# Kernel optimization log

Hardware: AMD Instinct MI355X
Metric: run time of the kernel (lower is better)

## Reference

```python
import jax, jax.numpy as jnp
import numpy as np

N = 100000     # total points
PBS = 500      # point_batch_size (hard-coded in module)
K = 100        # num_neighbors
KP = 15        # num_kernel_points
EPS = 1e-5


def _bn(x, g, b, axes):
    # torch BatchNorm in training mode: batch stats, biased variance
    m = jnp.mean(x, axis=axes, keepdims=True)
    v = jnp.var(x, axis=axes, keepdims=True)
    return (x - m) / jnp.sqrt(v + EPS) * g + b


def setup_inputs() -> dict:
    key = jax.random.key(0)
    ks = jax.random.split(key, 16)
    rn = lambda k, sh, s=1.0: jax.random.normal(k, sh, jnp.float32) * s
    return {
        "pts": rn(ks[0], (N, 3)),
        "normal": rn(ks[1], (N, 3)),
        "kp_points": rn(ks[2], (KP, 3)),
        "kp_weights": rn(ks[3], (KP, 3, 128), 0.3),
        "kp_sigma": jnp.float32(1.0),
        "conv1_w": rn(ks[4], (1024, 128), 128 ** -0.5),
        "conv1_b": rn(ks[5], (1024,), 0.02),
        "bn1_g": jnp.ones((1024,), jnp.float32),
        "bn1_b": jnp.zeros((1024,), jnp.float32),
        "fc1_w": rn(ks[6], (512, 1024), 1024 ** -0.5),
        "fc1_b": rn(ks[7], (512,), 0.02),
        "bn4_g": jnp.ones((512,), jnp.float32),
        "bn4_b": jnp.zeros((512,), jnp.float32),
        "fc2_w": rn(ks[8], (256, 512), 512 ** -0.5),
        "fc2_b": rn(ks[9], (256,), 0.02),
        "bn5_g": jnp.ones((256,), jnp.float32),
        "bn5_b": jnp.zeros((256,), jnp.float32),
        "fc3_w": rn(ks[10], (3, 256), 256 ** -0.5),
        "fc3_b": rn(ks[11], (3,), 0.02),
        "index": jax.random.randint(ks[12], (PBS,), 0, N, jnp.int32),
    }


def reference(pts, normal, kp_points, kp_weights, kp_sigma,
              conv1_w, conv1_b, bn1_g, bn1_b,
              fc1_w, fc1_b, bn4_g, bn4_b,
              fc2_w, fc2_b, bn5_g, bn5_b,
              fc3_w, fc3_b, index):
    sel = pts[index]                                               # [B,3]
    # L-inf pairwise distance and kNN (topk of -dist, as in the torch code)
    dist = jnp.max(jnp.abs(sel[:, None, :] - pts[None, :, :]), axis=-1)  # [B,N]
    _, nbr = jax.lax.top_k(-dist, K)                               # [B,K]
    rel = pts[nbr] - sel[:, None, :]                               # [B,K,3]

    # KPConv: gaussian weights vs kernel points, per-kernel-point linear map
    d2 = jnp.sum((rel[:, :, None, :] - kp_points[None, None]) ** 2, axis=-1)  # [B,K,KP]
    w = jnp.exp(-0.5 * d2 / (kp_sigma ** 2))
    wf = rel[:, :, None, :] * w[..., None]                         # [B,K,KP,3]
    h = jax.nn.relu(jnp.einsum('bnkc,kco->bno', wf, kp_weights))   # [B,K,128]

    # 1x1 conv 128->1024, relu then BN over (batch, points) per channel
    h = jnp.einsum('bnc,oc->bno', h, conv1_w) + conv1_b            # [B,K,1024]
    h = _bn(jax.nn.relu(h), bn1_g, bn1_b, (0, 1))
    feat = jnp.max(h, axis=1)                                      # [B,1024]

    feat = _bn(jax.nn.relu(feat @ fc1_w.T + fc1_b), bn4_g, bn4_b, (0,))
    feat = _bn(jax.nn.relu(feat @ fc2_w.T + fc2_b), bn5_g, bn5_b, (0,))
    feat = feat @ fc3_w.T + fc3_b                                  # [B,3]
    return feat, normal[index]
```

## Files before the change

kernel.cpp:

```cpp
#include <hip/hip_runtime.h>
#include <hip/hip_fp16.h>

#define NPTS 100000
#define NB 500
#define KNN 100
#define KPN 15
#define C1 128
#define C2 1024
#define C3 512
#define C4 256

#define G 64
#define NCELLS (G * G * G)
#define GB 5.0f
#define GINVH ((float)G / (2.f * GB))
#define CAND_CAP 2048

typedef _Float16 half8 __attribute__((ext_vector_type(8)));
typedef float f32x4 __attribute__((ext_vector_type(4)));

__device__ __forceinline__ int cell_coord(float x) {
  int c = (int)floorf((x + GB) * GINVH);
  return min(max(c, 0), G - 1);
}
__device__ __forceinline__ int cell_of(float x, float y, float z) {
  return (cell_coord(x) << 12) | (cell_coord(y) << 6) | cell_coord(z);
}

__global__ __launch_bounds__(256) void prep_kernel(
    const float* __restrict__ pts, const float* __restrict__ normal,
    const int* __restrict__ index, const float* __restrict__ w1,
    const float* __restrict__ kpw, const float* __restrict__ fc1w,
    const float* __restrict__ fc2w, float* __restrict__ sel,
    float* __restrict__ out2, __half* __restrict__ wh,
    __half* __restrict__ kpwT_hi, __half* __restrict__ kpwT_lo,
    __half* __restrict__ fwhi, __half* __restrict__ fwlo,
    __half* __restrict__ f2whi, __half* __restrict__ f2wlo,
    unsigned* __restrict__ cnt) {
  int i = blockIdx.x * 256 + threadIdx.x;
  if (i < NB) {
    int ix = index[i];
    sel[i * 3 + 0] = pts[3 * ix + 0];
    sel[i * 3 + 1] = pts[3 * ix + 1];
    sel[i * 3 + 2] = pts[3 * ix + 2];
    out2[i * 3 + 0] = normal[3 * ix + 0];
    out2[i * 3 + 1] = normal[3 * ix + 1];
    out2[i * 3 + 2] = normal[3 * ix + 2];
  }
  if (i < C2 * C1) wh[i] = __float2half(w1[i]);
  if (i < 128 * 64) {
    int o = i >> 6, j = i & 63;
    float v = (j < 45) ? kpw[j * 128 + o] : 0.f;
    __half hi = __float2half_rn(v);
    kpwT_hi[i] = hi;
    kpwT_lo[i] = __float2half_rn(v - __half2float(hi));
  }
  if (i < C3 * C2) {
    float v = fc1w[i];
    __half hi = __float2half_rn(v);
    fwhi[i] = hi;
    fwlo[i] = __float2half_rn(v - __half2float(hi));
  }
  if (i < C4 * C3) {
    float v = fc2w[i];
    __half hi = __float2half_rn(v);
    f2whi[i] = hi;
    f2wlo[i] = __float2half_rn(v - __half2float(hi));
  }
  if (i < NPTS)
    atomicAdd(&cnt[cell_of(pts[3 * i], pts[3 * i + 1], pts[3 * i + 2])], 1u);
}

__global__ __launch_bounds__(256) void grid_scan1_kernel(
    const unsigned* __restrict__ cnt, unsigned* __restrict__ cursor,
    unsigned* __restrict__ chunktot) {
  const int tid = threadIdx.x;
  int base = blockIdx.x * 1024 + tid * 4;
  unsigned c0 = cnt[base], c1 = cnt[base + 1], c2 = cnt[base + 2],
           c3 = cnt[base + 3];
  unsigned tot = c0 + c1 + c2 + c3;
  __shared__ unsigned sb[256];
  sb[tid] = tot;
  __syncthreads();
  for (int off = 1; off < 256; off <<= 1) {
    unsigned add = (tid >= off) ? sb[tid - off] : 0u;
    __syncthreads();
    sb[tid] += add;
    __syncthreads();
  }
  unsigned excl = sb[tid] - tot;
  cursor[base] = excl;
  cursor[base + 1] = excl + c0;
  cursor[base + 2] = excl + c0 + c1;
  cursor[base + 3] = excl + c0 + c1 + c2;
  if (tid == 255) chunktot[blockIdx.x] = sb[255];
}

__global__ __launch_bounds__(256) void grid_scan2_kernel(
    const unsigned* __restrict__ chunktot, unsigned* __restrict__ chunkoff) {
  const int tid = threadIdx.x;
  unsigned v = chunktot[tid];
  __shared__ unsigned sb[256];
  sb[tid] = v;
  __syncthreads();
  for (int off = 1; off < 256; off <<= 1) {
    unsigned add = (tid >= off) ? sb[tid - off] : 0u;
    __syncthreads();
    sb[tid] += add;
    __syncthreads();
  }
  chunkoff[tid] = sb[tid] - v;
}

__global__ __launch_bounds__(256) void grid_scan3_kernel(
    unsigned* __restrict__ cursor, const unsigned* __restrict__ chunkoff) {
  unsigned off = chunkoff[blockIdx.x];
  int base = blockIdx.x * 1024 + threadIdx.x * 4;
#pragma unroll
  for (int j = 0; j < 4; ++j) cursor[base + j] += off;
}

__global__ __launch_bounds__(256) void grid_scatter_kernel(
    const float* __restrict__ pts, unsigned* __restrict__ cursor,
    float4* __restrict__ sorted) {
  int i = blockIdx.x * 256 + threadIdx.x;
  if (i >= NPTS) return;
  float x = pts[3 * i], y = pts[3 * i + 1], z = pts[3 * i + 2];
  unsigned pos = atomicAdd(&cursor[cell_of(x, y, z)], 1u);
  sorted[pos] = make_float4(x, y, z, __int_as_float(i));
}

__device__ __forceinline__ unsigned linf_bits(float px, float py, float pz,
                                              float sx, float sy, float sz) {
  float dx = fabsf(px - sx), dy = fabsf(py - sy), dz = fabsf(pz - sz);
  return __float_as_uint(fmaxf(fmaxf(dx, dy), dz));
}

__global__ __launch_bounds__(256) void knn_kernel(
    const float4* __restrict__ sorted, const unsigned* __restrict__ cnt,
    const unsigned* __restrict__ cursor,
    const float* __restrict__ sel, int* __restrict__ nbr) {
  const int b = blockIdx.x;
  const int tid = threadIdx.x;
  __shared__ unsigned cbits[CAND_CAP];
  __shared__ int cidx[CAND_CAP];
  __shared__ unsigned hist[4096];
  __shared__ unsigned scanbuf[256];
  __shared__ int s_total, s_m, s_mc, s_chunk;
  __shared__ unsigned s_excl, s_bub;

  const float qx = sel[b * 3 + 0], qy = sel[b * 3 + 1], qz = sel[b * 3 + 2];
  const int qcx = cell_coord(qx), qcy = cell_coord(qy), qcz = cell_coord(qz);

  if (tid == 0) s_total = 0;
  __syncthreads();
  int s = 1;
  int pxlo = 1, pxhi = 0, pylo = 1, pyhi = 0, pzlo = 1, pzhi = 0;
  int xlo, xhi, ylo, yhi, zlo, zhi;
  for (;;) {
    xlo = max(qcx - s, 0); xhi = min(qcx + s, G - 1);
    ylo = max(qcy - s, 0); yhi = min(qcy + s, G - 1);
    zlo = max(qcz - s, 0); zhi = min(qcz + s, G - 1);
    int nx = xhi - xlo + 1, ny = yhi - ylo + 1, nz = zhi - zlo + 1;
    int ncell = nx * ny * nz;
    unsigned local = 0;
    for (int ci = tid; ci < ncell; ci += 256) {
      int cz = ci % nz;
      int r = ci / nz;
      int cy = r % ny;
      int cx = r / ny;
      int ax = xlo + cx, ay = ylo + cy, az = zlo + cz;
      if (ax >= pxlo && ax <= pxhi && ay >= pylo && ay <= pyhi &&
          az >= pzlo && az <= pzhi)
        continue;
      local += cnt[(ax << 12) | (ay << 6) | az];
    }
#pragma unroll
    for (int off = 32; off; off >>= 1) local += __shfl_down(local, off);
    if ((tid & 63) == 0) atomicAdd(&s_total, (int)local);
    __syncthreads();
    if (s_total >= KNN || (xlo == 0 && ylo == 0 && zlo == 0 && xhi == G - 1 &&
                           yhi == G - 1 && zhi == G - 1))
      break;
    pxlo = xlo; pxhi = xhi; pylo = ylo; pyhi = yhi; pzlo = zlo; pzhi = zhi;
    ++s;
    __syncthreads();
  }

  if (tid == 0) s_m = 0;
  __syncthreads();
  {
    int nx = xhi - xlo + 1, ny = yhi - ylo + 1, nz = zhi - zlo + 1;
    int ncell = nx * ny * nz;
    for (int ci = tid; ci < ncell; ci += 256) {
      int cz = ci % nz;
      int r = ci / nz;
      int cy = r % ny;
      int cx = r / ny;
      int cell = ((xlo + cx) << 12) | ((ylo + cy) << 6) | (zlo + cz);
      unsigned end = cursor[cell];
      unsigned beg = end - cnt[cell];
      int k = (int)(end - beg);
      if (k > 0) {
        int e0 = atomicAdd(&s_m, k);
        for (unsigned p = beg; p < end; ++p, ++e0) {
          if (e0 < CAND_CAP) {
            float4 f = sorted[p];
            cbits[e0] = linf_bits(f.x, f.y, f.z, qx, qy, qz);
            cidx[e0] = __float_as_int(f.w);
          }
        }
      }
    }
  }
  __syncthreads();
  int m = s_m < CAND_CAP ? s_m : CAND_CAP;

  for (int j = tid; j < 4096; j += 256) hist[j] = 0;
  __syncthreads();
  for (int e = tid; e < m; e += 256) atomicAdd(&hist[cbits[e] >> 19], 1u);
  __syncthreads();
  unsigned csum = 0;
  {
    int c0 = tid * 16;
#pragma unroll
    for (int j = 0; j < 16; ++j) csum += hist[c0 + j];
  }
  scanbuf[tid] = csum;
  __syncthreads();
  for (int off = 1; off < 256; off <<= 1) {
    unsigned add = (tid >= off) ? scanbuf[tid - off] : 0u;
    __syncthreads();
    scanbuf[tid] += add;
    __syncthreads();
  }
  {
    unsigned incl = scanbuf[tid], excl = incl - csum;
    if (excl < KNN && KNN <= incl) {
      s_chunk = tid;
      s_excl = excl;
    }
  }
  __syncthreads();
  if (tid == 0) {
    unsigned cum = s_excl;
    int bin = s_chunk * 16;
    while (cum + hist[bin] < KNN) {
      cum += hist[bin];
      ++bin;
    }
    s_bub = (unsigned)(bin + 1) << 19;
  }
  __syncthreads();

  const unsigned bub = s_bub;
  const float dub = __uint_as_float(bub);
  if (tid == 0) s_mc = 0;
  __syncthreads();
  {
    int xlo2 = min(max((int)floorf((qx - dub + GB) * GINVH), 0), G - 1);
    int xhi2 = min(max((int)floorf((qx + dub + GB) * GINVH), 0), G - 1);
    int ylo2 = min(max((int)floorf((qy - dub + GB) * GINVH), 0), G - 1);
    int yhi2 = min(max((int)floorf((qy + dub + GB) * GINVH), 0), G - 1);
    int zlo2 = min(max((int)floorf((qz - dub + GB) * GINVH), 0), G - 1);
    int zhi2 = min(max((int)floorf((qz + dub + GB) * GINVH), 0), G - 1);
    int nx = xhi2 - xlo2 + 1, ny = yhi2 - ylo2 + 1, nz = zhi2 - zlo2 + 1;
    int ncell = nx * ny * nz;
    for (int ci = tid; ci < ncell; ci += 256) {
      int cz = ci % nz;
      int r = ci / nz;
      int cy = r % ny;
      int cx = r / ny;
      int cell = ((xlo2 + cx) << 12) | ((ylo2 + cy) << 6) | (zlo2 + cz);
      unsigned end = cursor[cell];
      unsigned beg = end - cnt[cell];
      for (unsigned p = beg; p < end; ++p) {
        float4 f = sorted[p];
        unsigned bits = linf_bits(f.x, f.y, f.z, qx, qy, qz);
        if (bits < bub) {
          int e = atomicAdd(&s_mc, 1);
          if (e < CAND_CAP) {
            cbits[e] = bits;
            cidx[e] = __float_as_int(f.w);
          }
        }
      }
    }
  }
  __syncthreads();
  int mc = s_mc < CAND_CAP ? s_mc : CAND_CAP;

  for (int c = tid; c < mc; c += 256) {
    unsigned bc = cbits[c];
    int ic = cidx[c];
    int rank = 0;
    for (int j = 0; j < mc; ++j) {
      unsigned bj = cbits[j];
      rank += (bj < bc || (bj == bc && cidx[j] < ic)) ? 1 : 0;
    }
    if (rank < KNN) nbr[b * KNN + rank] = ic;
  }
}

__global__ __launch_bounds__(512, 2) void kpconv_conv1_kernel(
    const float* __restrict__ pts, const float* __restrict__ sel,
    const int* __restrict__ nbr, const float* __restrict__ kp_points,
    const __half* __restrict__ kpwT_hi, const __half* __restrict__ kpwT_lo,
    const float* __restrict__ kp_sigma, const __half* __restrict__ wh,
    const float* __restrict__ bias, float* __restrict__ featmax,
    float* __restrict__ featmin, float* __restrict__ featsum,
    float* __restrict__ featsq) {
  const int b = blockIdx.x;
  const int tid = threadIdx.x;
  const int wave = tid >> 6, lane = tid & 63;
  const int lr = lane & 15, quad = lane >> 4;

  __shared__ __align__(16) char smem[71168];
  __half* As_hi = (__half*)smem;
  __half* As_lo = As_hi + 112 * 72;
  __half* Bs_hi = As_lo + 112 * 72;
  __half* Bs_lo = Bs_hi + 128 * 72;
  float* rel = (float*)(Bs_lo + 128 * 72);
  float* kpp = rel + 100 * 4;
  __half* Hs = (__half*)smem;

  for (int i = tid; i < 128 * 8; i += 512) {
    int row = i >> 3, seg = i & 7;
    *(float4*)&Bs_hi[row * 72 + seg * 8] =
        *(const float4*)&kpwT_hi[row * 64 + seg * 8];
    *(float4*)&Bs_lo[row * 72 + seg * 8] =
        *(const float4*)&kpwT_lo[row * 64 + seg * 8];
  }
  {
    float4 z = make_float4(0.f, 0.f, 0.f, 0.f);
    for (int i = tid; i < 112 * 8; i += 512) {
      int row = i >> 3, seg = i & 7;
      *(float4*)&As_hi[row * 72 + seg * 8] = z;
      *(float4*)&As_lo[row * 72 + seg * 8] = z;
    }
  }
  if (tid < 45) kpp[tid] = kp_points[tid];
  if (tid < 100) {
    int idx = nbr[b * KNN + tid];
    rel[tid * 4 + 0] = pts[3 * idx + 0] - sel[b * 3 + 0];
    rel[tid * 4 + 1] = pts[3 * idx + 1] - sel[b * 3 + 1];
    rel[tid * 4 + 2] = pts[3 * idx + 2] - sel[b * 3 + 2];
  }
  __syncthreads();

  const float sg = kp_sigma[0];
  const float inv2s2 = -0.5f / (sg * sg);
  for (int i = tid; i < 100 * KPN; i += 512) {
    int k = i / KPN, p = i - k * KPN;
    float rx = rel[k * 4 + 0] - kpp[p * 3 + 0];
    float ry = rel[k * 4 + 1] - kpp[p * 3 + 1];
    float rz = rel[k * 4 + 2] - kpp[p * 3 + 2];
    float w = expf(inv2s2 * (rx * rx + ry * ry + rz * rz));
#pragma unroll
    for (int c = 0; c < 3; ++c) {
      float a = rel[k * 4 + c] * w;
      __half hi = __float2half_rn(a);
      As_hi[k * 72 + p * 3 + c] = hi;
      As_lo[k * 72 + p * 3 + c] = __float2half_rn(a - __half2float(hi));
    }
  }
  __syncthreads();

  f32x4 acc1[7];
#pragma unroll
  for (int m = 0; m < 7; ++m) acc1[m] = (f32x4)(0.f);
#pragma unroll
  for (int s = 0; s < 2; ++s) {
    int boff = (wave * 16 + lr) * 72 + s * 32 + quad * 8;
    half8 bhi = *(const half8*)&Bs_hi[boff];
    half8 blo = *(const half8*)&Bs_lo[boff];
#pragma unroll
    for (int m = 0; m < 7; ++m) {
      int aoff = (m * 16 + lr) * 72 + s * 32 + quad * 8;
      half8 ahi = *(const half8*)&As_hi[aoff];
      half8 alo = *(const half8*)&As_lo[aoff];
      acc1[m] = __builtin_amdgcn_mfma_f32_16x16x32_f16(ahi, bhi, acc1[m], 0, 0, 0);
      acc1[m] = __builtin_amdgcn_mfma_f32_16x16x32_f16(ahi, blo, acc1[m], 0, 0, 0);
      acc1[m] = __builtin_amdgcn_mfma_f32_16x16x32_f16(alo, bhi, acc1[m], 0, 0, 0);
    }
  }
  __syncthreads();

  {
    int col = wave * 16 + lr;
#pragma unroll
    for (int m = 0; m < 7; ++m)
#pragma unroll
      for (int r = 0; r < 4; ++r) {
        int row = m * 16 + quad * 4 + r;
        Hs[row * 136 + col] = __float2half_rn(fmaxf(acc1[m][r], 0.f));
      }
  }
  __syncthreads();

  half8 afr[4][7];
#pragma unroll
  for (int s = 0; s < 4; ++s)
#pragma unroll
    for (int m = 0; m < 7; ++m)
      afr[s][m] = *(const half8*)&Hs[(m * 16 + lr) * 136 + s * 32 + quad * 8];

  const int wrow = wave * 16 + lr;
  half8 bcur[4];
#pragma unroll
  for (int s = 0; s < 4; ++s)
    bcur[s] = *(const half8*)&wh[wrow * 128 + s * 32 + quad * 8];

  for (int c = 0; c < 8; ++c) {
    half8 bnxt[4];
    if (c + 1 < 8) {
#pragma unroll
      for (int s = 0; s < 4; ++s)
        bnxt[s] = *(const half8*)&wh[((c + 1) * 128 + wrow) * 128 + s * 32 +
                                     quad * 8];
    }

    f32x4 acc2[7];
#pragma unroll
    for (int m = 0; m < 7; ++m) acc2[m] = (f32x4)(0.f);
#pragma unroll
    for (int s = 0; s < 4; ++s)
#pragma unroll
      for (int m = 0; m < 7; ++m)
        acc2[m] = __builtin_amdgcn_mfma_f32_16x16x32_f16(afr[s][m], bcur[s],
                                                         acc2[m], 0, 0, 0);

    {
      int col = c * 128 + wrow;
      float bv = bias[col];
      float pmax = -1e30f, pmin = 1e30f, psum = 0.f, psq = 0.f;
#pragma unroll
      for (int m = 0; m < 7; ++m)
#pragma unroll
        for (int r = 0; r < 4; ++r) {
          int row = m * 16 + quad * 4 + r;
          if (row < 100) {
            float y = fmaxf(acc2[m][r] + bv, 0.f);
            pmax = fmaxf(pmax, y);
            pmin = fminf(pmin, y);
            psum += y;
            psq += y * y;
          }
        }
      pmax = fmaxf(pmax, __shfl_xor(pmax, 16));
      pmax = fmaxf(pmax, __shfl_xor(pmax, 32));
      pmin = fminf(pmin, __shfl_xor(pmin, 16));
      pmin = fminf(pmin, __shfl_xor(pmin, 32));
      psum += __shfl_xor(psum, 16);
      psum += __shfl_xor(psum, 32);
      psq += __shfl_xor(psq, 16);
      psq += __shfl_xor(psq, 32);
      if (quad == 0) {
        featmax[b * C2 + col] = pmax;
        featmin[b * C2 + col] = pmin;
        featsum[b * C2 + col] = psum;
        featsq[b * C2 + col] = psq;
      }
    }
#pragma unroll
    for (int s = 0; s < 4; ++s) bcur[s] = bnxt[s];
  }
}

__global__ __launch_bounds__(256) void stats1_kernel(
    const float* __restrict__ featsum, const float* __restrict__ featsq,
    float* __restrict__ bnsum, float* __restrict__ bnsq) {
  int col = blockIdx.x * 256 + threadIdx.x;
  int r0 = blockIdx.y * 50;
  float s = 0.f, q = 0.f;
  for (int r = r0; r < r0 + 50; ++r) {
    s += featsum[r * C2 + col];
    q += featsq[r * C2 + col];
  }
  atomicAdd(&bnsum[col], s);
  atomicAdd(&bnsq[col], q);
}

__global__ __launch_bounds__(256) void bn1half_kernel(
    const float* __restrict__ featmax, const float* __restrict__ featmin,
    const float* __restrict__ bnsum, const float* __restrict__ bnsq,
    const float* __restrict__ g, const float* __restrict__ bb,
    __half* __restrict__ Xhi, __half* __restrict__ Xlo) {
  int idx = blockIdx.x * 256 + threadIdx.x;
  if (idx >= NB * C2) return;
  int o = idx & (C2 - 1);
  const float invn = 1.f / (float)(NB * KNN);
  float m = bnsum[o] * invn;
  float v = bnsq[o] * invn - m * m;
  float a = g[o] / sqrtf(v + 1e-5f);
  float x = (a >= 0.f) ? featmax[idx] : featmin[idx];
  float y = (x - m) * a + bb[o];
  __half hi = __float2half_rn(y);
  Xhi[idx] = hi;
  Xlo[idx] = __float2half_rn(y - __half2float(hi));
}

__global__ __launch_bounds__(256) void fc1_mfma_kernel(
    const __half* __restrict__ Xhi, const __half* __restrict__ Xlo,
    const __half* __restrict__ Whi, const __half* __restrict__ Wlo,
    const float* __restrict__ bias, float* __restrict__ yraw,
    float* __restrict__ s, float* __restrict__ sq) {
  const int r0 = blockIdx.x * 64;
  const int n0 = blockIdx.y * 64;
  const int tid = threadIdx.x;
  const int wave = tid >> 6, lane = tid & 63;
  const int lr = lane & 15, quad = lane >> 4;
  __shared__ __half Xs_hi[64 * 72], Xs_lo[64 * 72];
  __shared__ __half Ws_hi[64 * 72], Ws_lo[64 * 72];

  f32x4 acc[4];
#pragma unroll
  for (int m = 0; m < 4; ++m) acc[m] = (f32x4)(0.f);

  for (int kc = 0; kc < C2; kc += 64) {
    __syncthreads();
    for (int i = tid; i < 64 * 8; i += 256) {
      int row = i >> 3, seg = i & 7;
      int gr = r0 + row;
      float4 vhi = make_float4(0.f, 0.f, 0.f, 0.f), vlo = vhi;
      if (gr < NB) {
        vhi = *(const float4*)&Xhi[gr * C2 + kc + seg * 8];
        vlo = *(const float4*)&Xlo[gr * C2 + kc + seg * 8];
      }
      *(float4*)&Xs_hi[row * 72 + seg * 8] = vhi;
      *(float4*)&Xs_lo[row * 72 + seg * 8] = vlo;
      *(float4*)&Ws_hi[row * 72 + seg * 8] =
          *(const float4*)&Whi[(n0 + row) * C2 + kc + seg * 8];
      *(float4*)&Ws_lo[row * 72 + seg * 8] =
          *(const float4*)&Wlo[(n0 + row) * C2 + kc + seg * 8];
    }
    __syncthreads();

#pragma unroll
    for (int s2 = 0; s2 < 2; ++s2) {
      int boff = (wave * 16 + lr) * 72 + s2 * 32 + quad * 8;
      half8 bhi = *(const half8*)&Ws_hi[boff];
      half8 blo = *(const half8*)&Ws_lo[boff];
#pragma unroll
      for (int m = 0; m < 4; ++m) {
        int aoff = (m * 16 + lr) * 72 + s2 * 32 + quad * 8;
        half8 ahi = *(const half8*)&Xs_hi[aoff];
        half8 alo = *(const half8*)&Xs_lo[aoff];
        acc[m] = __builtin_amdgcn_mfma_f32_16x16x32_f16(ahi, bhi, acc[m], 0, 0, 0);
        acc[m] = __builtin_amdgcn_mfma_f32_16x16x32_f16(ahi, blo, acc[m], 0, 0, 0);
        acc[m] = __builtin_amdgcn_mfma_f32_16x16x32_f16(alo, bhi, acc[m], 0, 0, 0);
      }
    }
  }

  {
    int col = n0 + wave * 16 + lr;
    float bv = bias[col];
    float psum = 0.f, psq = 0.f;
#pragma unroll
    for (int m = 0; m < 4; ++m)
#pragma unroll
      for (int r = 0; r < 4; ++r) {
        int row = r0 + m * 16 + quad * 4 + r;
        if (row < NB) {
          float y = fmaxf(acc[m][r] + bv, 0.f);
          yraw[row * C3 + col] = y;
          psum += y;
          psq += y * y;
        }
      }
    psum += __shfl_xor(psum, 16);
    psum += __shfl_xor(psum, 32);
    psq += __shfl_xor(psq, 16);
    psq += __shfl_xor(psq, 32);
    if (quad == 0) {
      atomicAdd(&s[col], psum);
      atomicAdd(&sq[col], psq);
    }
  }
}

__global__ __launch_bounds__(256) void fc2_mfma_kernel(
    const float* __restrict__ x,
    const float* __restrict__ bnsum4, const float* __restrict__ bnsq4,
    const float* __restrict__ g, const float* __restrict__ bb,
    const __half* __restrict__ Whi, const __half* __restrict__ Wlo,
    const float* __restrict__ bias, float* __restrict__ yraw,
    float* __restrict__ s, float* __restrict__ sq) {
  const int r0 = blockIdx.x * 64;
  const int n0 = blockIdx.y * 64;
  const int tid = threadIdx.x;
  const int wave = tid >> 6, lane = tid & 63;
  const int lr = lane & 15, quad = lane >> 4;
  __shared__ __half Xs_hi[64 * 72], Xs_lo[64 * 72];
  __shared__ __half Ws_hi[64 * 72], Ws_lo[64 * 72];
  __shared__ float amul[C3], badd[C3];

  {
    const float invn = 1.f / (float)NB;
    for (int o = tid; o < C3; o += 256) {
      float m = bnsum4[o] * invn;
      float v = bnsq4[o] * invn - m * m;
      float a = g[o] / sqrtf(v + 1e-5f);
      amul[o] = a;
      badd[o] = bb[o] - m * a;
    }
  }

  f32x4 acc[4];
#pragma unroll
  for (int m = 0; m < 4; ++m) acc[m] = (f32x4)(0.f);

  for (int kc = 0; kc < C3; kc += 64) {
    __syncthreads();
    for (int i = tid; i < 64 * 8; i += 256) {
      int row = i >> 3, seg = i & 7;
      int gr = r0 + row;
      __half hbuf[8], lbuf[8];
      if (gr < NB) {
        float4 a0 = *(const float4*)&x[gr * C3 + kc + seg * 8];
        float4 a1 = *(const float4*)&x[gr * C3 + kc + seg * 8 + 4];
        float vals[8] = {a0.x, a0.y, a0.z, a0.w, a1.x, a1.y, a1.z, a1.w};
#pragma unroll
        for (int j = 0; j < 8; ++j) {
          int o = kc + seg * 8 + j;
          float y = vals[j] * amul[o] + badd[o];
          __half hi = __float2half_rn(y);
          hbuf[j] = hi;
          lbuf[j] = __float2half_rn(y - __half2float(hi));
        }
      } else {
#pragma unroll
        for (int j = 0; j < 8; ++j) {
          hbuf[j] = __float2half_rn(0.f);
          lbuf[j] = __float2half_rn(0.f);
        }
      }
      *(float4*)&Xs_hi[row * 72 + seg * 8] = *(float4*)hbuf;
      *(float4*)&Xs_lo[row * 72 + seg * 8] = *(float4*)lbuf;
      *(float4*)&Ws_hi[row * 72 + seg * 8] =
          *(const float4*)&Whi[(n0 + row) * C3 + kc + seg * 8];
      *(float4*)&Ws_lo[row * 72 + seg * 8] =
          *(const float4*)&Wlo[(n0 + row) * C3 + kc + seg * 8];
    }
    __syncthreads();

#pragma unroll
    for (int s2 = 0; s2 < 2; ++s2) {
      int boff = (wave * 16 + lr) * 72 + s2 * 32 + quad * 8;
      half8 bhi = *(const half8*)&Ws_hi[boff];
      half8 blo = *(const half8*)&Ws_lo[boff];
#pragma unroll
      for (int m = 0; m < 4; ++m) {
        int aoff = (m * 16 + lr) * 72 + s2 * 32 + quad * 8;
        half8 ahi = *(const half8*)&Xs_hi[aoff];
        half8 alo = *(const half8*)&Xs_lo[aoff];
        acc[m] = __builtin_amdgcn_mfma_f32_16x16x32_f16(ahi, bhi, acc[m], 0, 0, 0);
        acc[m] = __builtin_amdgcn_mfma_f32_16x16x32_f16(ahi, blo, acc[m], 0, 0, 0);
        acc[m] = __builtin_amdgcn_mfma_f32_16x16x32_f16(alo, bhi, acc[m], 0, 0, 0);
      }
    }
  }

  {
    int col = n0 + wave * 16 + lr;
    float bv = bias[col];
    float psum = 0.f, psq = 0.f;
#pragma unroll
    for (int m = 0; m < 4; ++m)
#pragma unroll
      for (int r = 0; r < 4; ++r) {
        int row = r0 + m * 16 + quad * 4 + r;
        if (row < NB) {
          float y = fmaxf(acc[m][r] + bv, 0.f);
          yraw[row * C4 + col] = y;
          psum += y;
          psq += y * y;
        }
      }
    psum += __shfl_xor(psum, 16);
    psum += __shfl_xor(psum, 32);
    psq += __shfl_xor(psq, 16);
    psq += __shfl_xor(psq, 32);
    if (quad == 0) {
      atomicAdd(&s[col], psum);
      atomicAdd(&sq[col], psq);
    }
  }
}

__global__ __launch_bounds__(256) void fc3_kernel(
    const float* __restrict__ x,
    const float* __restrict__ bnsum, const float* __restrict__ bnsq,
    const float* __restrict__ g, const float* __restrict__ bb,
    const float* __restrict__ w, const float* __restrict__ bias,
    float* __restrict__ out) {
  const int tid = threadIdx.x;
  __shared__ float pmul[C4], padd[C4];
  {
    const float invn = 1.f / (float)NB;
    float m = bnsum[tid] * invn;
    float v = bnsq[tid] * invn - m * m;
    float a = g[tid] / sqrtf(v + 1e-5f);
    pmul[tid] = a;
    padd[tid] = bb[tid] - m * a;
  }
  __syncthreads();
  int idx = blockIdx.x * 256 + tid;
  if (idx >= NB * 3) return;
  int b = idx / 3, o = idx % 3;
  float acc = 0.f;
  for (int k = 0; k < C4; ++k)
    acc += (x[b * C4 + k] * pmul[k] + padd[k]) * w[o * C4 + k];
  out[idx] = acc + bias[o];
}

extern "C" void kernel_launch(void* const* d_in, const int* in_sizes, int n_in,
                              void* d_out, int out_size, void* d_ws,
                              size_t ws_size, hipStream_t stream) {
  const float* pts = (const float*)d_in[0];
  const float* normal = (const float*)d_in[1];
  const float* kp_points = (const float*)d_in[2];
  const float* kp_weights = (const float*)d_in[3];
  const float* kp_sigma = (const float*)d_in[4];
  const float* conv1_w = (const float*)d_in[5];
  const float* conv1_b = (const float*)d_in[6];
  const float* bn1_g = (const float*)d_in[7];
  const float* bn1_b = (const float*)d_in[8];
  const float* fc1_w = (const float*)d_in[9];
  const float* fc1_b = (const float*)d_in[10];
  const float* bn4_g = (const float*)d_in[11];
  const float* bn4_b = (const float*)d_in[12];
  const float* fc2_w = (const float*)d_in[13];
  const float* fc2_b = (const float*)d_in[14];
  const float* bn5_g = (const float*)d_in[15];
  const float* bn5_b = (const float*)d_in[16];
  const float* fc3_w = (const float*)d_in[17];
  const float* fc3_b = (const float*)d_in[18];
  const int* index = (const int*)d_in[19];
  float* out = (float*)d_out;

  char* p = (char*)d_ws;
  auto carve = [&](size_t bytes) {
    void* r = (void*)p;
    p += (bytes + 255) & ~(size_t)255;
    return r;
  };
  float* sel = (float*)carve(NB * 3 * 4);
  int* nbr = (int*)carve(NB * KNN * 4);
  __half* wh = (__half*)carve((size_t)C2 * C1 * 2);
  __half* kpwT_hi = (__half*)carve((size_t)128 * 64 * 2);
  __half* kpwT_lo = (__half*)carve((size_t)128 * 64 * 2);
  __half* fwhi = (__half*)carve((size_t)C3 * C2 * 2);
  __half* fwlo = (__half*)carve((size_t)C3 * C2 * 2);
  __half* f2whi = (__half*)carve((size_t)C4 * C3 * 2);
  __half* f2wlo = (__half*)carve((size_t)C4 * C3 * 2);
  __half* Xhi = (__half*)carve((size_t)NB * C2 * 2);
  __half* Xlo = (__half*)carve((size_t)NB * C2 * 2);
  float* featmax = (float*)carve(NB * C2 * 4);
  float* featmin = (float*)carve(NB * C2 * 4);
  float* featsum = (float*)carve(NB * C2 * 4);
  float* featsq = (float*)carve(NB * C2 * 4);
  float* f2raw = (float*)carve(NB * C3 * 4);
  float* f3raw = (float*)carve(NB * C4 * 4);
  float* stats = (float*)carve((2 * C2 + 2 * C3 + 2 * C4) * 4);
  float* bnsum = stats;
  float* bnsq = stats + C2;
  float* s4 = stats + 2 * C2;
  float* sq4 = s4 + C3;
  float* s5 = sq4 + C3;
  float* sq5 = s5 + C4;
  unsigned* cellcnt = (unsigned*)carve((size_t)NCELLS * 4);
  unsigned* cellcur = (unsigned*)carve((size_t)NCELLS * 4);
  unsigned* chunktot = (unsigned*)carve(256 * 4);
  unsigned* chunkoff = (unsigned*)carve(256 * 4);
  float4* sortedpts = (float4*)carve((size_t)NPTS * 16);

  hipMemsetAsync(stats, 0, (2 * C2 + 2 * C3 + 2 * C4) * 4, stream);
  hipMemsetAsync(cellcnt, 0, (size_t)NCELLS * 4, stream);

  prep_kernel<<<(C3 * C2 + 255) / 256, 256, 0, stream>>>(
      pts, normal, index, conv1_w, kp_weights, fc1_w, fc2_w, sel,
      out + NB * 3, wh, kpwT_hi, kpwT_lo, fwhi, fwlo, f2whi, f2wlo, cellcnt);
  grid_scan1_kernel<<<256, 256, 0, stream>>>(cellcnt, cellcur, chunktot);
  grid_scan2_kernel<<<1, 256, 0, stream>>>(chunktot, chunkoff);
  grid_scan3_kernel<<<256, 256, 0, stream>>>(cellcur, chunkoff);
  grid_scatter_kernel<<<(NPTS + 255) / 256, 256, 0, stream>>>(pts, cellcur,
                                                              sortedpts);
  knn_kernel<<<NB, 256, 0, stream>>>(sortedpts, cellcnt, cellcur, sel, nbr);
  kpconv_conv1_kernel<<<NB, 512, 0, stream>>>(
      pts, sel, nbr, kp_points, kpwT_hi, kpwT_lo, kp_sigma, wh, conv1_b,
      featmax, featmin, featsum, featsq);
  stats1_kernel<<<dim3(4, 10), 256, 0, stream>>>(featsum, featsq, bnsum,
                                                 bnsq);
  bn1half_kernel<<<(NB * C2 + 255) / 256, 256, 0, stream>>>(
      featmax, featmin, bnsum, bnsq, bn1_g, bn1_b, Xhi, Xlo);
  fc1_mfma_kernel<<<dim3(8, 8), 256, 0, stream>>>(Xhi, Xlo, fwhi, fwlo, fc1_b,
                                                  f2raw, s4, sq4);
  fc2_mfma_kernel<<<dim3(8, 4), 256, 0, stream>>>(
      f2raw, s4, sq4, bn4_g, bn4_b, f2whi, f2wlo, fc2_b, f3raw, s5, sq5);
  fc3_kernel<<<(NB * 3 + 255) / 256, 256, 0, stream>>>(
      f3raw, s5, sq5, bn5_g, bn5_b, fc3_w, fc3_b, out);
}
```

Measured before the change: 261.9 us.

## Merge grid scan kernels via atomic block bases and skip redundant kNN rescan

The three-kernel prefix scan over grid cells becomes a single kernel. Each block claims its global base offset with an atomicAdd on a zeroed counter, so cell ranges stay contiguous even though blocks no longer land in cell order. In the kNN kernel, the second candidate-gathering pass is skipped when the refined cell box lies inside the first-pass box and the first-pass candidate list did not overflow, reusing those candidates. This removes two kernel launches and the repeated global-memory point scans, at the cost of relying on the first-pass candidate buffers still being valid.

```diff
diff --git a/kernel.cpp b/kernel.cpp
--- a/kernel.cpp
+++ b/kernel.cpp
@@ -71,15 +71,16 @@
     atomicAdd(&cnt[cell_of(pts[3 * i], pts[3 * i + 1], pts[3 * i + 2])], 1u);
 }
 
-__global__ __launch_bounds__(256) void grid_scan1_kernel(
+__global__ __launch_bounds__(256) void grid_scan_kernel(
     const unsigned* __restrict__ cnt, unsigned* __restrict__ cursor,
-    unsigned* __restrict__ chunktot) {
+    unsigned* __restrict__ gbase) {
   const int tid = threadIdx.x;
   int base = blockIdx.x * 1024 + tid * 4;
   unsigned c0 = cnt[base], c1 = cnt[base + 1], c2 = cnt[base + 2],
            c3 = cnt[base + 3];
   unsigned tot = c0 + c1 + c2 + c3;
   __shared__ unsigned sb[256];
+  __shared__ unsigned s_base;
   sb[tid] = tot;
   __syncthreads();
   for (int off = 1; off < 256; off <<= 1) {
@@ -88,36 +89,13 @@
     sb[tid] += add;
     __syncthreads();
   }
-  unsigned excl = sb[tid] - tot;
+  if (tid == 255) s_base = atomicAdd(gbase, sb[255]);
+  __syncthreads();
+  unsigned excl = s_base + sb[tid] - tot;
   cursor[base] = excl;
   cursor[base + 1] = excl + c0;
   cursor[base + 2] = excl + c0 + c1;
   cursor[base + 3] = excl + c0 + c1 + c2;
-  if (tid == 255) chunktot[blockIdx.x] = sb[255];
-}
-
-__global__ __launch_bounds__(256) void grid_scan2_kernel(
-    const unsigned* __restrict__ chunktot, unsigned* __restrict__ chunkoff) {
-  const int tid = threadIdx.x;
-  unsigned v = chunktot[tid];
-  __shared__ unsigned sb[256];
-  sb[tid] = v;
-  __syncthreads();
-  for (int off = 1; off < 256; off <<= 1) {
-    unsigned add = (tid >= off) ? sb[tid - off] : 0u;
-    __syncthreads();
-    sb[tid] += add;
-    __syncthreads();
-  }
-  chunkoff[tid] = sb[tid] - v;
-}
-
-__global__ __launch_bounds__(256) void grid_scan3_kernel(
-    unsigned* __restrict__ cursor, const unsigned* __restrict__ chunkoff) {
-  unsigned off = chunkoff[blockIdx.x];
-  int base = blockIdx.x * 1024 + threadIdx.x * 4;
-#pragma unroll
-  for (int j = 0; j < 4; ++j) cursor[base + j] += off;
 }
 
 __global__ __launch_bounds__(256) void grid_scatter_kernel(
@@ -255,40 +233,48 @@
 
   const unsigned bub = s_bub;
   const float dub = __uint_as_float(bub);
-  if (tid == 0) s_mc = 0;
-  __syncthreads();
-  {
-    int xlo2 = min(max((int)floorf((qx - dub + GB) * GINVH), 0), G - 1);
-    int xhi2 = min(max((int)floorf((qx + dub + GB) * GINVH), 0), G - 1);
-    int ylo2 = min(max((int)floorf((qy - dub + GB) * GINVH), 0), G - 1);
-    int yhi2 = min(max((int)floorf((qy + dub + GB) * GINVH), 0), G - 1);
-    int zlo2 = min(max((int)floorf((qz - dub + GB) * GINVH), 0), G - 1);
-    int zhi2 = min(max((int)floorf((qz + dub + GB) * GINVH), 0), G - 1);
-    int nx = xhi2 - xlo2 + 1, ny = yhi2 - ylo2 + 1, nz = zhi2 - zlo2 + 1;
-    int ncell = nx * ny * nz;
-    for (int ci = tid; ci < ncell; ci += 256) {
-      int cz = ci % nz;
-      int r = ci / nz;
-      int cy = r % ny;
-      int cx = r / ny;
-      int cell = ((xlo2 + cx) << 12) | ((ylo2 + cy) << 6) | (zlo2 + cz);
-      unsigned end = cursor[cell];
-      unsigned beg = end - cnt[cell];
-      for (unsigned p = beg; p < end; ++p) {
-        float4 f = sorted[p];
-        unsigned bits = linf_bits(f.x, f.y, f.z, qx, qy, qz);
-        if (bits < bub) {
-          int e = atomicAdd(&s_mc, 1);
-          if (e < CAND_CAP) {
-            cbits[e] = bits;
-            cidx[e] = __float_as_int(f.w);
+  int xlo2 = min(max((int)floorf((qx - dub + GB) * GINVH), 0), G - 1);
+  int xhi2 = min(max((int)floorf((qx + dub + GB) * GINVH), 0), G - 1);
+  int ylo2 = min(max((int)floorf((qy - dub + GB) * GINVH), 0), G - 1);
+  int yhi2 = min(max((int)floorf((qy + dub + GB) * GINVH), 0), G - 1);
+  int zlo2 = min(max((int)floorf((qz - dub + GB) * GINVH), 0), G - 1);
+  int zhi2 = min(max((int)floorf((qz + dub + GB) * GINVH), 0), G - 1);
+  const bool nested = (s_m <= CAND_CAP) && xlo2 >= xlo && xhi2 <= xhi &&
+                      ylo2 >= ylo && yhi2 <= yhi && zlo2 >= zlo && zhi2 <= zhi;
+
+  int mc;
+  if (nested) {
+    mc = m;
+  } else {
+    if (tid == 0) s_mc = 0;
+    __syncthreads();
+    {
+      int nx = xhi2 - xlo2 + 1, ny = yhi2 - ylo2 + 1, nz = zhi2 - zlo2 + 1;
+      int ncell = nx * ny * nz;
+      for (int ci = tid; ci < ncell; ci += 256) {
+        int cz = ci % nz;
+        int r = ci / nz;
+        int cy = r % ny;
+        int cx = r / ny;
+        int cell = ((xlo2 + cx) << 12) | ((ylo2 + cy) << 6) | (zlo2 + cz);
+        unsigned end = cursor[cell];
+        unsigned beg = end - cnt[cell];
+        for (unsigned p = beg; p < end; ++p) {
+          float4 f = sorted[p];
+          unsigned bits = linf_bits(f.x, f.y, f.z, qx, qy, qz);
+          if (bits < bub) {
+            int e = atomicAdd(&s_mc, 1);
+            if (e < CAND_CAP) {
+              cbits[e] = bits;
+              cidx[e] = __float_as_int(f.w);
+            }
           }
         }
       }
     }
-  }
-  __syncthreads();
-  int mc = s_mc < CAND_CAP ? s_mc : CAND_CAP;
+    __syncthreads();
+    mc = s_mc < CAND_CAP ? s_mc : CAND_CAP;
+  }
 
   for (int c = tid; c < mc; c += 256) {
     unsigned bc = cbits[c];
@@ -763,28 +749,25 @@
   float* featsq = (float*)carve(NB * C2 * 4);
   float* f2raw = (float*)carve(NB * C3 * 4);
   float* f3raw = (float*)carve(NB * C4 * 4);
-  float* stats = (float*)carve((2 * C2 + 2 * C3 + 2 * C4) * 4);
+  float* stats = (float*)carve((2 * C2 + 2 * C3 + 2 * C4 + 64) * 4);
   float* bnsum = stats;
   float* bnsq = stats + C2;
   float* s4 = stats + 2 * C2;
   float* sq4 = s4 + C3;
   float* s5 = sq4 + C3;
   float* sq5 = s5 + C4;
+  unsigned* gbase = (unsigned*)(stats + 2 * C2 + 2 * C3 + 2 * C4);
   unsigned* cellcnt = (unsigned*)carve((size_t)NCELLS * 4);
   unsigned* cellcur = (unsigned*)carve((size_t)NCELLS * 4);
-  unsigned* chunktot = (unsigned*)carve(256 * 4);
-  unsigned* chunkoff = (unsigned*)carve(256 * 4);
   float4* sortedpts = (float4*)carve((size_t)NPTS * 16);
 
-  hipMemsetAsync(stats, 0, (2 * C2 + 2 * C3 + 2 * C4) * 4, stream);
+  hipMemsetAsync(stats, 0, (2 * C2 + 2 * C3 + 2 * C4 + 64) * 4, stream);
   hipMemsetAsync(cellcnt, 0, (size_t)NCELLS * 4, stream);
 
   prep_kernel<<<(C3 * C2 + 255) / 256, 256, 0, stream>>>(
       pts, normal, index, conv1_w, kp_weights, fc1_w, fc2_w, sel,
       out + NB * 3, wh, kpwT_hi, kpwT_lo, fwhi, fwlo, f2whi, f2wlo, cellcnt);
-  grid_scan1_kernel<<<256, 256, 0, stream>>>(cellcnt, cellcur, chunktot);
-  grid_scan2_kernel<<<1, 256, 0, stream>>>(chunktot, chunkoff);
-  grid_scan3_kernel<<<256, 256, 0, stream>>>(cellcur, chunkoff);
+  grid_scan_kernel<<<256, 256, 0, stream>>>(cellcnt, cellcur, gbase);
   grid_scatter_kernel<<<(NPTS + 255) / 256, 256, 0, stream>>>(pts, cellcur,
                                                               sortedpts);
   knn_kernel<<<NB, 256, 0, stream>>>(sortedpts, cellcnt, cellcur, sel, nbr);
```

Result: slower. 366.8 us (+40.0%).
